# Performance work log

Measured on AMD Instinct MI355X. Metric: run time of the kernel, lower is better.

Reference implementation:

```python
import jax, jax.numpy as jnp
import numpy as np

W_PROFILE, W_PLANFORM, W_MEAN = 0.5, 0.3, 0.2
CELL_SIZE = 10.0
EPS = 1e-08


def _kernels():
    sobel_x = np.array([[-1, 0, 1], [-2, 0, 2], [-1, 0, 1]], np.float32) / 8.0
    sobel_y = np.array([[-1, -2, -1], [0, 0, 0], [1, 2, 1]], np.float32) / 8.0
    k_xx = np.array([[1, -2, 1], [1, -2, 1], [1, -2, 1]], np.float32) / 3.0
    k_yy = np.array([[1, 1, 1], [-2, -2, -2], [1, 1, 1]], np.float32) / 3.0
    k_xy = np.array([[-1, 0, 1], [0, 0, 0], [1, 0, -1]], np.float32) / 4.0
    # stack into one [5,1,3,3] OIHW kernel -> single fused conv for all 5 stencils
    return jnp.asarray(np.stack([sobel_x, sobel_y, k_xx, k_xy, k_yy])[:, None])

_K = _kernels()


def _curvatures(dem):
    # dem: [B,1,H,W] -> derivatives p,q,r,s,t each [B,1,H,W]
    d = jax.lax.conv_general_dilated(dem, _K, window_strides=(1, 1), padding='SAME',
                                     dimension_numbers=('NCHW', 'OIHW', 'NCHW'))
    p = d[:, 0:1] / CELL_SIZE
    q = d[:, 1:2] / CELL_SIZE
    r = d[:, 2:3] / CELL_SIZE ** 2
    s = d[:, 3:4] / CELL_SIZE ** 2
    t = d[:, 4:5] / CELL_SIZE ** 2
    p2, q2, pq = p * p, q * q, p * q
    denom1 = p2 + q2
    denom2 = (1 + denom1) ** 1.5
    profile = (r * p2 + 2 * s * pq + t * q2) / (denom1 * jnp.sqrt(1 + denom1) + EPS)
    planform = (r * q2 - 2 * s * pq + t * p2) / (denom1 ** 1.5 + EPS)
    mean = ((1 + q2) * r - 2 * pq * s + (1 + p2) * t) / (2 * denom2 + EPS)
    flat = denom1 < EPS
    profile = jnp.where(flat, 0.0, profile)
    planform = jnp.where(flat, 0.0, planform)
    return profile, planform, mean


def setup_inputs() -> dict:
    key = jax.random.key(0)
    k1, k2 = jax.random.split(key)
    shape = (16, 1, 1024, 1024)
    return {
        'pred': jax.random.normal(k1, shape, dtype=jnp.float32),
        'target': jax.random.normal(k2, shape, dtype=jnp.float32),
    }


def reference(pred, target):
    pp, pl, pm = _curvatures(pred)
    tp, tl, tm = _curvatures(target)
    loss_profile = jnp.mean(jnp.abs(pp - tp))
    loss_planform = jnp.mean(jnp.abs(pl - tl))
    loss_mean = jnp.mean(jnp.abs(pm - tm))
    return W_PROFILE * loss_profile + W_PLANFORM * loss_planform + W_MEAN * loss_mean
```

## Files before the change

### kernel.cpp

```cpp
#include <hip/hip_runtime.h>
#include <math.h>


constexpr int IMG_B = 16;
constexpr int IMG_H = 1024;
constexpr int IMG_W = 1024;
constexpr int ROWS  = 16;
constexpr int BLOCK = 256;
constexpr int COLS_T = 2;
constexpr int TILE_W = BLOCK * COLS_T;
constexpr int TILES_X = IMG_W / TILE_W;
constexpr int TILES_Y = IMG_H / ROWS;
constexpr int NBLOCKS = IMG_B * TILES_Y * TILES_X;
constexpr float EPS = 1e-8f;

constexpr float A2 = 1.0f / 6400.0f;
constexpr float Bc = 1.0f / 300.0f;
constexpr float C2 = 1.0f / 200.0f;

typedef float f2v __attribute__((ext_vector_type(2)));
typedef float f4v __attribute__((ext_vector_type(4), aligned(4)));

__device__ __forceinline__ f2v pk_fma(f2v a, f2v b, f2v c) {
    return __builtin_elementwise_fma(a, b, c);
}

struct Row { f2v hx, hs, rs; };

template<bool TILE0>
__device__ __forceinline__ void prep_row(const float* __restrict__ Abase, int y,
                                         bool edge, Row& o)
{
    if ((unsigned)y < (unsigned)IMG_H) {
        const f4v L = *reinterpret_cast<const f4v*>(Abase + ((size_t)y << 10));
        float w0, w1, w2, w3;
        if (TILE0) {
            w0 = edge ? 0.0f : L.x;
            w1 = edge ? L.x  : L.y;
            w2 = edge ? L.y  : L.z;
            w3 = edge ? L.z  : L.w;
        } else {
            w0 = edge ? L.y  : L.x;
            w1 = edge ? L.z  : L.y;
            w2 = edge ? L.w  : L.z;
            w3 = edge ? 0.0f : L.w;
        }
        const f2v lo = {w0, w1};
        const f2v mid = {w1, w2};
        const f2v hi = {w2, w3};
        const f2v e = lo + hi;
        o.hx = hi - lo;
        o.hs = pk_fma(f2v{2.0f, 2.0f}, mid, e);
        o.rs = e + mid;
    } else {
        o.hx = f2v{0.0f, 0.0f}; o.hs = f2v{0.0f, 0.0f}; o.rs = f2v{0.0f, 0.0f};
    }
}

__device__ __forceinline__ void curv(const Row& a, const Row& b, const Row& c,
                                     f2v& prof, f2v& plan, f2v& mean2)
{
    const f2v A2f = {A2, A2}, Bcf = {Bc, Bc}, C2f = {C2, C2};
    const f2v m3  = {-3.0f, -3.0f};

    const f2v gx  = pk_fma(f2v{2.0f, 2.0f}, b.hx, a.hx + c.hx);
    const f2v gy  = c.hs - a.hs;
    const f2v tot = (a.rs + c.rs) + b.rs;
    const f2v H   = (a.hs + c.hs) + b.hs;
    const f2v rxx = pk_fma(m3, H - tot, tot);
    const f2v tyy = pk_fma(m3, b.rs, tot);
    const f2v sxy = a.hx - c.hx;

    const f2v gx2 = gx * gx, gy2 = gy * gy, gxgy = gx * gy;
    const f2v g2  = gx2 + gy2;
    const f2v d1  = A2f * g2;
    const f2v od  = d1 + f2v{1.0f, 1.0f};

    f2v rsq_od, sq_d1;
    rsq_od.x = __builtin_amdgcn_rsqf(od.x);
    rsq_od.y = __builtin_amdgcn_rsqf(od.y);
    sq_d1.x  = __builtin_amdgcn_sqrtf(d1.x);
    sq_d1.y  = __builtin_amdgcn_sqrtf(d1.y);
    const f2v sq_od = od * rsq_od;

    const f2v h1    = pk_fma(tyy, gy2, rxx * gx2);
    const f2v h3    = pk_fma(tyy, gx2, rxx * gy2);
    const f2v h2c   = C2f * (sxy * gxgy);
    const f2v nprof = A2f * pk_fma(Bcf, h1, h2c);
    const f2v nplan = A2f * pk_fma(Bcf, h3, -h2c);
    const f2v mnum  = pk_fma(Bcf, rxx + tyy, nplan);

    const f2v den_p = pk_fma(d1, sq_od, f2v{EPS, EPS});
    const f2v den_l = pk_fma(d1, sq_d1, f2v{EPS, EPS});
    const f2v plprod = den_p * den_l;
    f2v rcpPL;
    rcpPL.x = __builtin_amdgcn_rcpf(plprod.x);
    rcpPL.y = __builtin_amdgcn_rcpf(plprod.y);

    prof  = (nprof * den_l) * rcpPL;
    plan  = (nplan * den_p) * rcpPL;
    mean2 = mnum * ((rsq_od * rsq_od) * rsq_od);
    prof.x = (d1.x < EPS) ? 0.0f : prof.x;
    prof.y = (d1.y < EPS) ? 0.0f : prof.y;
    plan.x = (d1.x < EPS) ? 0.0f : plan.x;
    plan.y = (d1.y < EPS) ? 0.0f : plan.y;
}

template<bool TILE0>
__device__ __forceinline__ f2v run_tile(const float* __restrict__ P,
                                        const float* __restrict__ T,
                                        int y0, bool edge)
{
    const f2v w05 = {0.5f, 0.5f}, w03 = {0.3f, 0.3f}, w01 = {0.1f, 0.1f};
    Row pr[3], tr[3];
    prep_row<TILE0>(P, y0 - 1, edge, pr[0]);
    prep_row<TILE0>(T, y0 - 1, edge, tr[0]);
    prep_row<TILE0>(P, y0,     edge, pr[1]);
    prep_row<TILE0>(T, y0,     edge, tr[1]);

    f2v acc = {0.0f, 0.0f};
#pragma unroll
    for (int i = 0; i < ROWS; ++i) {
        const int ia = i % 3, ib = (i + 1) % 3, ic = (i + 2) % 3;
        prep_row<TILE0>(P, y0 + i + 1, edge, pr[ic]);
        prep_row<TILE0>(T, y0 + i + 1, edge, tr[ic]);
        f2v pp, pl, pm, qp, ql, qm;
        curv(pr[ia], pr[ib], pr[ic], pp, pl, pm);
        curv(tr[ia], tr[ib], tr[ic], qp, ql, qm);
        acc = pk_fma(w05, __builtin_elementwise_abs(pp - qp), acc);
        acc = pk_fma(w03, __builtin_elementwise_abs(pl - ql), acc);
        acc = pk_fma(w01, __builtin_elementwise_abs(pm - qm), acc);
    }
    return acc;
}

__global__ __launch_bounds__(BLOCK) void curv_loss_main(
    const float* __restrict__ pred, const float* __restrict__ targ,
    float* __restrict__ blocksums)
{
    const int tid = threadIdx.x;
    const int b   = blockIdx.x;
    const int tx  = b & (TILES_X - 1);
    const int ty  = (b >> 1) & (TILES_Y - 1);
    const int img = b >> 7;
    const int y0  = ty * ROWS;
    const int x0  = tx * TILE_W + COLS_T * tid;

    int cload = x0 - 1;
    bool edge;
    if (tx == 0) { edge = (cload < 0);          if (edge) cload = 0; }
    else         { edge = (cload > IMG_W - 4);  if (edge) cload = IMG_W - 4; }

    const size_t base = (size_t)img * (size_t)(IMG_H * IMG_W) + cload;
    const float* __restrict__ P = pred + base;
    const float* __restrict__ T = targ + base;

    const f2v accv = (tx == 0) ? run_tile<true >(P, T, y0, edge)
                               : run_tile<false>(P, T, y0, edge);
    float a = accv.x + accv.y;

#pragma unroll
    for (int off = 32; off > 0; off >>= 1) a += __shfl_down(a, off, 64);
    __shared__ float ws[BLOCK / 64];
    const int lane = tid & 63, wid = tid >> 6;
    if (lane == 0) ws[wid] = a;
    __syncthreads();
    if (tid == 0)
        blocksums[b] = (ws[0] + ws[1]) + (ws[2] + ws[3]);
}

__global__ __launch_bounds__(BLOCK) void curv_loss_final(
    const float* __restrict__ blocksums, float* __restrict__ out)
{
    const int tid = threadIdx.x;
    float v = 0.0f;
#pragma unroll
    for (int i = 0; i < NBLOCKS / BLOCK; ++i) v += blocksums[i * BLOCK + tid];
#pragma unroll
    for (int off = 32; off > 0; off >>= 1) v += __shfl_down(v, off, 64);
    __shared__ float ws[BLOCK / 64];
    const int lane = tid & 63, wid = tid >> 6;
    if (lane == 0) ws[wid] = v;
    __syncthreads();
    if (tid == 0) {
        const float tot = (ws[0] + ws[1]) + (ws[2] + ws[3]);
        out[0] = tot * (1.0f / (float)(IMG_B * IMG_H * IMG_W));
    }
}

extern "C" void kernel_launch(void* const* d_in, const int* in_sizes, int n_in,
                              void* d_out, int out_size, void* d_ws, size_t ws_size,
                              hipStream_t stream)
{
    const float* pred = (const float*)d_in[0];
    const float* targ = (const float*)d_in[1];
    float* out = (float*)d_out;
    float* blocksums = (float*)d_ws;

    curv_loss_main<<<NBLOCKS, BLOCK, 0, stream>>>(pred, targ, blocksums);
    curv_loss_final<<<1, BLOCK, 0, stream>>>(blocksums, out);
}
```

Measured before the change: 157.0 us.

## Pack pred/target into packed-math lanes with one column per thread

Changes the work split so each thread handles one column instead of two, and the packed f2v lanes now hold pred and target values for the same pixel rather than two adjacent columns. Each row is fetched with three scalar loads per tensor (left, center, right) instead of one unaligned 4-wide load, and the grid doubles. This removes the edge-shuffle selects and lets the abs-difference run on lane x versus lane y. The cost is more load instructions, with neighbouring threads re-reading the same cache lines, plus twice as many blocks and reductions.

```diff
diff --git a/kernel.cpp b/kernel.cpp
--- a/kernel.cpp
+++ b/kernel.cpp
@@ -7,9 +7,7 @@
 constexpr int IMG_W = 1024;
 constexpr int ROWS  = 16;
 constexpr int BLOCK = 256;
-constexpr int COLS_T = 2;
-constexpr int TILE_W = BLOCK * COLS_T;
-constexpr int TILES_X = IMG_W / TILE_W;
+constexpr int TILES_X = IMG_W / BLOCK;
 constexpr int TILES_Y = IMG_H / ROWS;
 constexpr int NBLOCKS = IMG_B * TILES_Y * TILES_X;
 constexpr float EPS = 1e-8f;
@@ -19,51 +17,21 @@
 constexpr float C2 = 1.0f / 200.0f;
 
 typedef float f2v __attribute__((ext_vector_type(2)));
-typedef float f4v __attribute__((ext_vector_type(4), aligned(4)));
 
 __device__ __forceinline__ f2v pk_fma(f2v a, f2v b, f2v c) {
     return __builtin_elementwise_fma(a, b, c);
 }
 
-struct Row { f2v hx, hs, rs; };
+struct Rowv { f2v hx, hs, rs; };
 
-template<bool TILE0>
-__device__ __forceinline__ void prep_row(const float* __restrict__ Abase, int y,
-                                         bool edge, Row& o)
-{
-    if ((unsigned)y < (unsigned)IMG_H) {
-        const f4v L = *reinterpret_cast<const f4v*>(Abase + ((size_t)y << 10));
-        float w0, w1, w2, w3;
-        if (TILE0) {
-            w0 = edge ? 0.0f : L.x;
-            w1 = edge ? L.x  : L.y;
-            w2 = edge ? L.y  : L.z;
-            w3 = edge ? L.z  : L.w;
-        } else {
-            w0 = edge ? L.y  : L.x;
-            w1 = edge ? L.z  : L.y;
-            w2 = edge ? L.w  : L.z;
-            w3 = edge ? 0.0f : L.w;
-        }
-        const f2v lo = {w0, w1};
-        const f2v mid = {w1, w2};
-        const f2v hi = {w2, w3};
-        const f2v e = lo + hi;
-        o.hx = hi - lo;
-        o.hs = pk_fma(f2v{2.0f, 2.0f}, mid, e);
-        o.rs = e + mid;
-    } else {
-        o.hx = f2v{0.0f, 0.0f}; o.hs = f2v{0.0f, 0.0f}; o.rs = f2v{0.0f, 0.0f};
-    }
-}
-
-__device__ __forceinline__ void curv(const Row& a, const Row& b, const Row& c,
-                                     f2v& prof, f2v& plan, f2v& mean2)
+__device__ __forceinline__ void curv_pair(const Rowv& a, const Rowv& b, const Rowv& c,
+                                          f2v& prof, f2v& plan, f2v& mean2)
 {
     const f2v A2f = {A2, A2}, Bcf = {Bc, Bc}, C2f = {C2, C2};
-    const f2v m3  = {-3.0f, -3.0f};
+    const f2v m3  = {-3.0f, -3.0f}, two = {2.0f, 2.0f};
+    const f2v epsf = {EPS, EPS};
 
-    const f2v gx  = pk_fma(f2v{2.0f, 2.0f}, b.hx, a.hx + c.hx);
+    const f2v gx  = pk_fma(two, b.hx, a.hx + c.hx);
     const f2v gy  = c.hs - a.hs;
     const f2v tot = (a.rs + c.rs) + b.rs;
     const f2v H   = (a.hs + c.hs) + b.hs;
@@ -86,12 +54,12 @@
     const f2v h1    = pk_fma(tyy, gy2, rxx * gx2);
     const f2v h3    = pk_fma(tyy, gx2, rxx * gy2);
     const f2v h2c   = C2f * (sxy * gxgy);
-    const f2v nprof = A2f * pk_fma(Bcf, h1, h2c);
+    const f2v nprof = A2f * pk_fma(Bcf, h1,  h2c);
     const f2v nplan = A2f * pk_fma(Bcf, h3, -h2c);
     const f2v mnum  = pk_fma(Bcf, rxx + tyy, nplan);
 
-    const f2v den_p = pk_fma(d1, sq_od, f2v{EPS, EPS});
-    const f2v den_l = pk_fma(d1, sq_d1, f2v{EPS, EPS});
+    const f2v den_p = pk_fma(d1, sq_od, epsf);
+    const f2v den_l = pk_fma(d1, sq_d1, epsf);
     const f2v plprod = den_p * den_l;
     f2v rcpPL;
     rcpPL.x = __builtin_amdgcn_rcpf(plprod.x);
@@ -106,34 +74,6 @@
     plan.y = (d1.y < EPS) ? 0.0f : plan.y;
 }
 
-template<bool TILE0>
-__device__ __forceinline__ f2v run_tile(const float* __restrict__ P,
-                                        const float* __restrict__ T,
-                                        int y0, bool edge)
-{
-    const f2v w05 = {0.5f, 0.5f}, w03 = {0.3f, 0.3f}, w01 = {0.1f, 0.1f};
-    Row pr[3], tr[3];
-    prep_row<TILE0>(P, y0 - 1, edge, pr[0]);
-    prep_row<TILE0>(T, y0 - 1, edge, tr[0]);
-    prep_row<TILE0>(P, y0,     edge, pr[1]);
-    prep_row<TILE0>(T, y0,     edge, tr[1]);
-
-    f2v acc = {0.0f, 0.0f};
-#pragma unroll
-    for (int i = 0; i < ROWS; ++i) {
-        const int ia = i % 3, ib = (i + 1) % 3, ic = (i + 2) % 3;
-        prep_row<TILE0>(P, y0 + i + 1, edge, pr[ic]);
-        prep_row<TILE0>(T, y0 + i + 1, edge, tr[ic]);
-        f2v pp, pl, pm, qp, ql, qm;
-        curv(pr[ia], pr[ib], pr[ic], pp, pl, pm);
-        curv(tr[ia], tr[ib], tr[ic], qp, ql, qm);
-        acc = pk_fma(w05, __builtin_elementwise_abs(pp - qp), acc);
-        acc = pk_fma(w03, __builtin_elementwise_abs(pl - ql), acc);
-        acc = pk_fma(w01, __builtin_elementwise_abs(pm - qm), acc);
-    }
-    return acc;
-}
-
 __global__ __launch_bounds__(BLOCK) void curv_loss_main(
     const float* __restrict__ pred, const float* __restrict__ targ,
     float* __restrict__ blocksums)
@@ -141,29 +81,63 @@
     const int tid = threadIdx.x;
     const int b   = blockIdx.x;
     const int tx  = b & (TILES_X - 1);
-    const int ty  = (b >> 1) & (TILES_Y - 1);
-    const int img = b >> 7;
+    const int ty  = (b >> 2) & (TILES_Y - 1);
+    const int img = b >> 8;
     const int y0  = ty * ROWS;
-    const int x0  = tx * TILE_W + COLS_T * tid;
+    const int x   = tx * BLOCK + tid;
 
-    int cload = x0 - 1;
-    bool edge;
-    if (tx == 0) { edge = (cload < 0);          if (edge) cload = 0; }
-    else         { edge = (cload > IMG_W - 4);  if (edge) cload = IMG_W - 4; }
+    const size_t ibase = (size_t)img * (size_t)(IMG_H * IMG_W);
+    const char* __restrict__ Pc = (const char*)(pred + ibase);
+    const char* __restrict__ Tc = (const char*)(targ + ibase);
 
-    const size_t base = (size_t)img * (size_t)(IMG_H * IMG_W) + cload;
-    const float* __restrict__ P = pred + base;
-    const float* __restrict__ T = targ + base;
+    const bool xm = (x > 0);
+    const bool xp = (x < IMG_W - 1);
+    const int eL = (x + (xm ? -1 : 0)) << 2;
+    const int eC = x << 2;
+    const int eR = (x + (xp ? +1 : 0)) << 2;
 
-    const f2v accv = (tx == 0) ? run_tile<true >(P, T, y0, edge)
-                               : run_tile<false>(P, T, y0, edge);
-    float a = accv.x + accv.y;
+    auto prep = [&](int y, Rowv& o) {
+        if ((unsigned)y < (unsigned)IMG_H) {
+            const int vo = y << 12;
+            const float pl = *(const float*)(Pc + vo + eL);
+            const float tl = *(const float*)(Tc + vo + eL);
+            const float pc = *(const float*)(Pc + vo + eC);
+            const float tc = *(const float*)(Tc + vo + eC);
+            const float pr = *(const float*)(Pc + vo + eR);
+            const float tr = *(const float*)(Tc + vo + eR);
+            const f2v w0 = {xm ? pl : 0.0f, xm ? tl : 0.0f};
+            const f2v w1 = {pc, tc};
+            const f2v w2 = {xp ? pr : 0.0f, xp ? tr : 0.0f};
+            const f2v e = w0 + w2;
+            o.hx = w2 - w0;
+            o.hs = pk_fma(f2v{2.0f, 2.0f}, w1, e);
+            o.rs = e + w1;
+        } else {
+            o.hx = f2v{0.0f, 0.0f}; o.hs = f2v{0.0f, 0.0f}; o.rs = f2v{0.0f, 0.0f};
+        }
+    };
+
+    Rowv w[3];
+    prep(y0 - 1, w[0]);
+    prep(y0,     w[1]);
+
+    float acc = 0.0f;
+#pragma unroll
+    for (int i = 0; i < ROWS; ++i) {
+        const int ia = i % 3, ib = (i + 1) % 3, ic = (i + 2) % 3;
+        prep(y0 + i + 1, w[ic]);
+        f2v prof, plan, mean2;
+        curv_pair(w[ia], w[ib], w[ic], prof, plan, mean2);
+        acc = fmaf(0.5f, fabsf(prof.x  - prof.y),  acc);
+        acc = fmaf(0.3f, fabsf(plan.x  - plan.y),  acc);
+        acc = fmaf(0.1f, fabsf(mean2.x - mean2.y), acc);
+    }
 
 #pragma unroll
-    for (int off = 32; off > 0; off >>= 1) a += __shfl_down(a, off, 64);
+    for (int off = 32; off > 0; off >>= 1) acc += __shfl_down(acc, off, 64);
     __shared__ float ws[BLOCK / 64];
     const int lane = tid & 63, wid = tid >> 6;
-    if (lane == 0) ws[wid] = a;
+    if (lane == 0) ws[wid] = acc;
     __syncthreads();
     if (tid == 0)
         blocksums[b] = (ws[0] + ws[1]) + (ws[2] + ws[3]);
```

Result: faster. 153.8 us (-2.0%).
